# Optimization experiments

Measured on AMD Instinct MI355X. Metric: run time of the kernel, lower is better.

Reference implementation:

```python
import jax, jax.numpy as jnp
import numpy as np

N_QUBITS = 4
DIM = 1 << N_QUBITS  # 16


def _apply1(state, gate, q):
    # state: [B, 16] complex; gate: [2,2] or [B,2,2]; q: qubit index (0 = MSB)
    B = state.shape[0]
    left = 1 << q
    right = 1 << (N_QUBITS - q - 1)
    s = state.reshape(B, left, 2, right)
    if gate.ndim == 2:
        out = jnp.einsum('ij,bajc->baic', gate, s)
    else:
        out = jnp.einsum('bij,bajc->baic', gate, s)
    return out.reshape(B, DIM)


def _cnot(state, c, t):
    # flip target axis where control bit == 1
    B = state.shape[0]
    s = state.reshape((B,) + (2,) * N_QUBITS)
    s0 = jax.lax.index_in_dim(s, 0, c + 1, keepdims=True)
    s1 = jax.lax.index_in_dim(s, 1, c + 1, keepdims=True)
    s1 = jnp.flip(s1, axis=t + 1)
    return jnp.concatenate([s0, s1], axis=c + 1).reshape(B, DIM)


def _ry(theta):
    # theta: [B] -> [B,2,2] complex
    c = jnp.cos(theta / 2)
    s = jnp.sin(theta / 2)
    g = jnp.stack([jnp.stack([c, -s], -1), jnp.stack([s, c], -1)], -2)
    return g.astype(jnp.complex64)


def _rz(theta):
    e0 = jnp.exp(-1j * theta.astype(jnp.complex64) / 2)
    e1 = jnp.exp(1j * theta.astype(jnp.complex64) / 2)
    z = jnp.zeros_like(e0)
    return jnp.stack([jnp.stack([e0, z], -1), jnp.stack([z, e1], -1)], -2)


def _u3(theta, phi, lam):
    # scalar params -> [2,2] complex
    th = theta.astype(jnp.complex64)
    ph = phi.astype(jnp.complex64)
    la = lam.astype(jnp.complex64)
    c = jnp.cos(th / 2)
    s = jnp.sin(th / 2)
    return jnp.array([[1.0, 0.0], [0.0, 0.0]], jnp.complex64) * c \
        + jnp.array([[0.0, -1.0], [0.0, 0.0]], jnp.complex64) * (jnp.exp(1j * la) * s) \
        + jnp.array([[0.0, 0.0], [1.0, 0.0]], jnp.complex64) * (jnp.exp(1j * ph) * s) \
        + jnp.array([[0.0, 0.0], [0.0, 1.0]], jnp.complex64) * (jnp.exp(1j * (ph + la)) * c)


_H = (jnp.array([[1.0, 1.0], [1.0, -1.0]], jnp.float32) / np.sqrt(2.0)).astype(jnp.complex64)


def _circuit(ry_ang, rz_ang, u3_params):
    # ry_ang, rz_ang: [B, 4]; u3_params: [4, 3]
    B = ry_ang.shape[0]
    state = jnp.zeros((B, DIM), jnp.complex64).at[:, 0].set(1.0)
    for q in range(N_QUBITS):
        state = _apply1(state, _H, q)
    for q in range(N_QUBITS):
        state = _apply1(state, _ry(ry_ang[:, q]), q)
    for q in range(N_QUBITS):
        state = _apply1(state, _rz(rz_ang[:, q]), q)
    for q in range(N_QUBITS):  # cnot_ring step=1
        state = _cnot(state, q, (q + 1) % N_QUBITS)
    for q in range(N_QUBITS):  # cnot_ring step=2
        state = _cnot(state, q, (q + 2) % N_QUBITS)
    for q in range(N_QUBITS):
        state = _apply1(state, _u3(u3_params[q, 0], u3_params[q, 1], u3_params[q, 2]), q)
    # Z expectations on each wire
    probs = jnp.abs(state) ** 2  # [B, 16]
    probs = probs.reshape((B,) + (2,) * N_QUBITS)
    exps = []
    for q in range(N_QUBITS):
        axes = tuple(a for a in range(1, N_QUBITS + 1) if a != q + 1)
        p = jnp.sum(probs, axis=axes)  # [B, 2]
        exps.append(p[:, 0] - p[:, 1])
    return jnp.stack(exps, axis=1)  # [B, 4]


def setup_inputs() -> dict:
    key = jax.random.key(0)
    k = jax.random.split(key, 6)
    B = 32768
    input_features = jax.random.normal(k[0], (B, 512), jnp.float32)
    pre_w = jax.random.normal(k[1], (N_QUBITS, 512), jnp.float32) / np.sqrt(512.0)
    pre_b = jnp.zeros((N_QUBITS,), jnp.float32)
    u3_params = jax.random.uniform(k[2], (N_QUBITS, 3), jnp.float32, 0.0, 2.0 * np.pi)
    post_w = jax.random.normal(k[3], (2, N_QUBITS), jnp.float32) / np.sqrt(float(N_QUBITS))
    post_b = jnp.zeros((2,), jnp.float32)
    return {"input_features": input_features, "pre_w": pre_w, "pre_b": pre_b,
            "u3_params": u3_params, "post_w": post_w, "post_b": post_b}


def reference(input_features, pre_w, pre_b, u3_params, post_w, post_b):
    pre_out = input_features @ pre_w.T + pre_b              # [B, 4]
    q_in = jnp.tanh(pre_out / 10.0) * (np.pi / 2.0)          # [B, 4]
    ry_ang = jnp.arctan(q_in)
    rz_ang = jnp.arctan(q_in * q_in)
    q_out = _circuit(ry_ang, rz_ang, u3_params)              # [B, 4] real
    return q_out @ post_w.T + post_b                         # [B, 2]
```

## Files before the change

### kernel.cpp

```cpp
#include <hip/hip_runtime.h>
#include <math.h>

#define NQ 4
#define DIM 16
#define K 512

__global__ __launch_bounds__(256) void qnet_fused(const float* __restrict__ x,
                                                  const float* __restrict__ w,
                                                  const float* __restrict__ bias,
                                                  const float* __restrict__ u3p,
                                                  const float* __restrict__ post_w,
                                                  const float* __restrict__ post_b,
                                                  float* __restrict__ out,
                                                  int B) {
    __shared__ float lds_pre[64];

    const int wave = (int)(threadIdx.x >> 6);
    const int lane = (int)(threadIdx.x & 63);
    const int block_row0 = (int)blockIdx.x * 16;
    const int row0 = block_row0 + wave * 4;

    if (row0 < B) {
        float4 wf[NQ][2];
#pragma unroll
        for (int q = 0; q < NQ; ++q) {
#pragma unroll
            for (int h = 0; h < 2; ++h)
                wf[q][h] = *(const float4*)(w + q * K + h * 256 + lane * 4);
        }

        float acc[4][NQ];
#pragma unroll
        for (int r = 0; r < 4; ++r) {
            int row = row0 + r;
            if (row >= B) row = B - 1;
            const float* xr = x + (size_t)row * K;
            float4 x0 = *(const float4*)(xr + lane * 4);
            float4 x1 = *(const float4*)(xr + 256 + lane * 4);
#pragma unroll
            for (int q = 0; q < NQ; ++q) {
                acc[r][q] = x0.x * wf[q][0].x + x0.y * wf[q][0].y
                          + x0.z * wf[q][0].z + x0.w * wf[q][0].w
                          + x1.x * wf[q][1].x + x1.y * wf[q][1].y
                          + x1.z * wf[q][1].z + x1.w * wf[q][1].w;
            }
        }

        const int l1 = lane & 1;
        const int l2 = lane & 2;
        float v[4];
#pragma unroll
        for (int r = 0; r < 4; ++r) {
            float a01k = l1 ? acc[r][1] : acc[r][0];
            float a01s = l1 ? acc[r][0] : acc[r][1];
            a01k += __shfl_xor(a01s, 1, 64);
            float a23k = l1 ? acc[r][3] : acc[r][2];
            float a23s = l1 ? acc[r][2] : acc[r][3];
            a23k += __shfl_xor(a23s, 1, 64);
            float vk = l2 ? a23k : a01k;
            float vs = l2 ? a01k : a23k;
            vk += __shfl_xor(vs, 2, 64);
#pragma unroll
            for (int off = 4; off <= 32; off <<= 1)
                vk += __shfl_xor(vk, off, 64);
            v[r] = vk;
        }

        if (lane < 16) {
            const int r = lane >> 2;
            const int q = lane & 3;
            float vr = (r == 0) ? v[0] : (r == 1) ? v[1] : (r == 2) ? v[2] : v[3];
            lds_pre[wave * 16 + lane] = vr + bias[q];
        }
    }
    __syncthreads();

    const int t = (int)threadIdx.x;
    if (t >= 16) return;
    const int b = block_row0 + t;
    if (b >= B) return;

    float pre[NQ] = {lds_pre[t * 4 + 0], lds_pre[t * 4 + 1],
                     lds_pre[t * 4 + 2], lds_pre[t * 4 + 3]};

    float ry[NQ], rz[NQ];
#pragma unroll
    for (int q = 0; q < NQ; ++q) {
        float z = pre[q] * 0.1f;
        float tnh = 1.0f - 2.0f / (__expf(2.0f * z) + 1.0f);
        float qi = tnh * 1.5707963267948966f;
        ry[q] = atanf(qi);
        rz[q] = atanf(qi * qi);
    }

    float sr[DIM], si[DIM];
#pragma unroll
    for (int i = 0; i < DIM; ++i) { sr[i] = 0.25f; si[i] = 0.0f; }

#pragma unroll
    for (int q = 0; q < NQ; ++q) {
        float c, s;
        __sincosf(ry[q] * 0.5f, &s, &c);
        const int m = 1 << (3 - q);
#pragma unroll
        for (int i = 0; i < DIM; ++i) {
            if (i & m) continue;
            const int j = i | m;
            float r0 = sr[i], i0 = si[i], r1 = sr[j], i1 = si[j];
            sr[i] = c * r0 - s * r1;  si[i] = c * i0 - s * i1;
            sr[j] = s * r0 + c * r1;  si[j] = s * i0 + c * i1;
        }
    }

#pragma unroll
    for (int q = 0; q < NQ; ++q) {
        float c, s;
        __sincosf(rz[q] * 0.5f, &s, &c);
        const int m = 1 << (3 - q);
#pragma unroll
        for (int i = 0; i < DIM; ++i) {
            const float sg = (i & m) ? s : -s;
            float r = sr[i], im = si[i];
            sr[i] = c * r - sg * im;
            si[i] = c * im + sg * r;
        }
    }

    const int cn_c[8] = {0, 1, 2, 3, 0, 1, 2, 3};
    const int cn_t[8] = {1, 2, 3, 0, 2, 3, 0, 1};
#pragma unroll
    for (int k = 0; k < 8; ++k) {
        const int cm = 1 << (3 - cn_c[k]);
        const int tm = 1 << (3 - cn_t[k]);
#pragma unroll
        for (int i = 0; i < DIM; ++i) {
            if ((i & cm) && !(i & tm)) {
                const int j = i | tm;
                float tr = sr[i]; sr[i] = sr[j]; sr[j] = tr;
                float ti = si[i]; si[i] = si[j]; si[j] = ti;
            }
        }
    }

#pragma unroll
    for (int q = 0; q < NQ; ++q) {
        float th = u3p[q * 3 + 0], ph = u3p[q * 3 + 1], la = u3p[q * 3 + 2];
        float ct, st, cl, sl, cp, sp, cpl, spl;
        __sincosf(th * 0.5f, &st, &ct);
        __sincosf(la, &sl, &cl);
        __sincosf(ph, &sp, &cp);
        __sincosf(ph + la, &spl, &cpl);
        const float g01r = -cl * st, g01i = -sl * st;
        const float g10r = cp * st,  g10i = sp * st;
        const float g11r = cpl * ct, g11i = spl * ct;
        const int m = 1 << (3 - q);
#pragma unroll
        for (int i = 0; i < DIM; ++i) {
            if (i & m) continue;
            const int j = i | m;
            float r0 = sr[i], i0 = si[i], r1 = sr[j], i1 = si[j];
            sr[i] = ct * r0 + g01r * r1 - g01i * i1;
            si[i] = ct * i0 + g01r * i1 + g01i * r1;
            sr[j] = g10r * r0 - g10i * i0 + g11r * r1 - g11i * i1;
            si[j] = g10r * i0 + g10i * r0 + g11r * i1 + g11i * r1;
        }
    }

    float ex[NQ] = {0.f, 0.f, 0.f, 0.f};
#pragma unroll
    for (int i = 0; i < DIM; ++i) {
        const float p2 = sr[i] * sr[i] + si[i] * si[i];
#pragma unroll
        for (int q = 0; q < NQ; ++q)
            ex[q] += (i & (1 << (3 - q))) ? -p2 : p2;
    }

    float o0 = post_b[0], o1 = post_b[1];
#pragma unroll
    for (int q = 0; q < NQ; ++q) {
        o0 += ex[q] * post_w[q];
        o1 += ex[q] * post_w[4 + q];
    }
    *(float2*)(out + (size_t)b * 2) = make_float2(o0, o1);
}

extern "C" void kernel_launch(void* const* d_in, const int* in_sizes, int n_in,
                              void* d_out, int out_size, void* d_ws, size_t ws_size,
                              hipStream_t stream) {
    const float* x      = (const float*)d_in[0];
    const float* pre_w  = (const float*)d_in[1];
    const float* pre_b  = (const float*)d_in[2];
    const float* u3p    = (const float*)d_in[3];
    const float* post_w = (const float*)d_in[4];
    const float* post_b = (const float*)d_in[5];
    float* out = (float*)d_out;

    const int B = in_sizes[0] / K;

    const int rows_per_block = 16;
    const int blocks = (B + rows_per_block - 1) / rows_per_block;
    qnet_fused<<<blocks, 256, 0, stream>>>(x, pre_w, pre_b, u3p, post_w, post_b, out, B);
}
```

Before: 102.7 us.

## Process 64 rows per block with software-prefetched row loop per wave

Each wave now handles 16 input rows instead of 4, so each block covers 64 rows and the circuit simulation phase uses 64 threads instead of 16. The row loop prefetches the next row's x vectors while reducing the current one, which overlaps global loads with the shuffle reduction. Weight loads are amortized over more rows, and the grid has a quarter as many blocks. In exchange, only one row's loads are in flight at a time instead of four, so memory-level parallelism per wave may drop, and there are fewer blocks to spread across CUs.

```diff
diff --git a/kernel.cpp b/kernel.cpp
--- a/kernel.cpp
+++ b/kernel.cpp
@@ -4,6 +4,8 @@
 #define NQ 4
 #define DIM 16
 #define K 512
+#define RPB 64
+#define RPW 16
 
 __global__ __launch_bounds__(256) void qnet_fused(const float* __restrict__ x,
                                                   const float* __restrict__ w,
@@ -13,14 +15,14 @@
                                                   const float* __restrict__ post_b,
                                                   float* __restrict__ out,
                                                   int B) {
-    __shared__ float lds_pre[64];
+    __shared__ float lds_pre[RPB * 4];
 
     const int wave = (int)(threadIdx.x >> 6);
     const int lane = (int)(threadIdx.x & 63);
-    const int block_row0 = (int)blockIdx.x * 16;
-    const int row0 = block_row0 + wave * 4;
-
-    if (row0 < B) {
+    const int block_row0 = (int)blockIdx.x * RPB;
+    const int row0 = block_row0 + wave * RPW;
+
+    {
         float4 wf[NQ][2];
 #pragma unroll
         for (int q = 0; q < NQ; ++q) {
@@ -29,33 +31,38 @@
                 wf[q][h] = *(const float4*)(w + q * K + h * 256 + lane * 4);
         }
 
-        float acc[4][NQ];
-#pragma unroll
-        for (int r = 0; r < 4; ++r) {
-            int row = row0 + r;
-            if (row >= B) row = B - 1;
-            const float* xr = x + (size_t)row * K;
-            float4 x0 = *(const float4*)(xr + lane * 4);
-            float4 x1 = *(const float4*)(xr + 256 + lane * 4);
-#pragma unroll
-            for (int q = 0; q < NQ; ++q) {
-                acc[r][q] = x0.x * wf[q][0].x + x0.y * wf[q][0].y
-                          + x0.z * wf[q][0].z + x0.w * wf[q][0].w
-                          + x1.x * wf[q][1].x + x1.y * wf[q][1].y
-                          + x1.z * wf[q][1].z + x1.w * wf[q][1].w;
-            }
-        }
-
         const int l1 = lane & 1;
         const int l2 = lane & 2;
-        float v[4];
-#pragma unroll
-        for (int r = 0; r < 4; ++r) {
-            float a01k = l1 ? acc[r][1] : acc[r][0];
-            float a01s = l1 ? acc[r][0] : acc[r][1];
+
+        int rc = row0; if (rc > B - 1) rc = B - 1;
+        const float* xr = x + (size_t)rc * K;
+        float4 xa0 = *(const float4*)(xr + lane * 4);
+        float4 xa1 = *(const float4*)(xr + 256 + lane * 4);
+
+#pragma unroll
+        for (int r = 0; r < RPW; ++r) {
+            float4 xb0, xb1;
+            if (r + 1 < RPW) {
+                int rn = row0 + r + 1; if (rn > B - 1) rn = B - 1;
+                const float* xn = x + (size_t)rn * K;
+                xb0 = *(const float4*)(xn + lane * 4);
+                xb1 = *(const float4*)(xn + 256 + lane * 4);
+            }
+
+            float a[NQ];
+#pragma unroll
+            for (int q = 0; q < NQ; ++q) {
+                a[q] = xa0.x * wf[q][0].x + xa0.y * wf[q][0].y
+                     + xa0.z * wf[q][0].z + xa0.w * wf[q][0].w
+                     + xa1.x * wf[q][1].x + xa1.y * wf[q][1].y
+                     + xa1.z * wf[q][1].z + xa1.w * wf[q][1].w;
+            }
+
+            float a01k = l1 ? a[1] : a[0];
+            float a01s = l1 ? a[0] : a[1];
             a01k += __shfl_xor(a01s, 1, 64);
-            float a23k = l1 ? acc[r][3] : acc[r][2];
-            float a23s = l1 ? acc[r][2] : acc[r][3];
+            float a23k = l1 ? a[3] : a[2];
+            float a23s = l1 ? a[2] : a[3];
             a23k += __shfl_xor(a23s, 1, 64);
             float vk = l2 ? a23k : a01k;
             float vs = l2 ? a01k : a23k;
@@ -63,25 +70,22 @@
 #pragma unroll
             for (int off = 4; off <= 32; off <<= 1)
                 vk += __shfl_xor(vk, off, 64);
-            v[r] = vk;
-        }
-
-        if (lane < 16) {
-            const int r = lane >> 2;
-            const int q = lane & 3;
-            float vr = (r == 0) ? v[0] : (r == 1) ? v[1] : (r == 2) ? v[2] : v[3];
-            lds_pre[wave * 16 + lane] = vr + bias[q];
+
+            if (lane < 4)
+                lds_pre[(wave * RPW + r) * 4 + lane] = vk;
+
+            xa0 = xb0; xa1 = xb1;
         }
     }
     __syncthreads();
 
     const int t = (int)threadIdx.x;
-    if (t >= 16) return;
+    if (t >= RPB) return;
     const int b = block_row0 + t;
     if (b >= B) return;
 
-    float pre[NQ] = {lds_pre[t * 4 + 0], lds_pre[t * 4 + 1],
-                     lds_pre[t * 4 + 2], lds_pre[t * 4 + 3]};
+    const float4 pv = *(const float4*)(&lds_pre[t * 4]);
+    float pre[NQ] = {pv.x + bias[0], pv.y + bias[1], pv.z + bias[2], pv.w + bias[3]};
 
     float ry[NQ], rz[NQ];
 #pragma unroll
@@ -197,7 +201,6 @@
 
     const int B = in_sizes[0] / K;
 
-    const int rows_per_block = 16;
-    const int blocks = (B + rows_per_block - 1) / rows_per_block;
+    const int blocks = (B + RPB - 1) / RPB;
     qnet_fused<<<blocks, 256, 0, stream>>>(x, pre_w, pre_b, u3p, post_w, post_b, out, B);
 }
```

Measured after the change: 104.4 us. No clear change (+1.6%).
